# Performance work log

Measured on AMD Instinct MI355X. Metric: run time of the kernel, lower is better.

## Reference

```python
import jax, jax.numpy as jnp
import numpy as np

N, D = 8192, 4096


def setup_inputs() -> dict:
    key = jax.random.key(0)
    k1, k2, k3 = jax.random.split(key, 3)
    x = jax.random.normal(k1, (N, D), jnp.float32)
    W = jax.random.normal(k2, (D, D), jnp.float32) / np.sqrt(D)  # nn.Linear weight [out,in]
    b = jax.random.normal(k3, (D,), jnp.float32) * 0.01
    recency_weight = jnp.full((1,), -0.1, jnp.float32)
    return {"x": x, "W": W, "b": b, "recency_weight": recency_weight}


def reference(x, W, b, recency_weight):
    # linear -> relu projection
    x_proj = jax.nn.relu(x @ W.T + b)  # [N, D]
    # self-similarity
    scores = x_proj @ x_proj.T  # [N, N]
    n = scores.shape[0]
    idx = jnp.arange(n)
    # triu mask with diagonal=0 (use_current_timestep=False): keep strictly lower triangle
    mask = idx[None, :] >= idx[:, None]
    scores = jnp.where(mask, -jnp.inf, scores)
    # recency bias: toeplitz(arange(n)) == |i - j|, zeroed on masked positions
    rec = jnp.abs(idx[:, None] - idx[None, :]).astype(scores.dtype)
    rec = jnp.where(mask, 0.0, rec)
    scores = scores + recency_weight[0] * rec
    # row 0 is fully masked (-inf everywhere); replace with finite values to avoid
    # NaN in softmax -- the row is overwritten with zeros afterwards anyway.
    scores = scores.at[0].set(0.0)
    attn = jax.nn.softmax(scores, axis=1)
    attn = attn.at[0].set(0.0)  # matches scores[0] = zeros in the torch code
    return attn
```

## Files before the change

kernel.cpp:

```cpp
#include <hip/hip_runtime.h>
#include <hip/hip_bf16.h>
#include <stdint.h>

typedef _Float16 f16_t;
typedef f16_t f16x8_t __attribute__((ext_vector_type(8)));
typedef f16_t f16x4_t __attribute__((ext_vector_type(4)));
typedef float f32x4_t __attribute__((ext_vector_type(4)));

#define NROWS 8192
#define DDIM  4096
#define BK 32
#define KTILES (DDIM / BK)
#define LSTR 40

__device__ __forceinline__ void gload16(const void* g, void* s) {
  __builtin_amdgcn_global_load_lds(
      (const __attribute__((address_space(1))) void*)g,
      (__attribute__((address_space(3))) void*)s, 16, 0, 0);
}

__global__ __launch_bounds__(256) void k_split(const float* __restrict__ in,
                                               f16_t* __restrict__ hi,
                                               f16_t* __restrict__ lo) {
  const long i = ((long)blockIdx.x * 256 + threadIdx.x) * 4;
  const float4 v = *reinterpret_cast<const float4*>(in + i);
  float vv[4] = {v.x, v.y, v.z, v.w};
  f16x4_t h, l;
#pragma unroll
  for (int c = 0; c < 4; ++c) {
    f16_t hh = (f16_t)vv[c];
    h[c] = hh;
    l[c] = (f16_t)(vv[c] - (float)hh);
  }
  *reinterpret_cast<f16x4_t*>(hi + i) = h;
  *reinterpret_cast<f16x4_t*>(lo + i) = l;
}

typedef f16_t lds4_t[4][256][BK];

__device__ __forceinline__ void gemm_core256_3p(
    const f16_t* __restrict__ pAh, const f16_t* __restrict__ pAl, long lda,
    const f16_t* __restrict__ pBh, const f16_t* __restrict__ pBl, long ldb,
    lds4_t* sm, f32x4_t (&acc)[8][4]) {
  const int t = threadIdx.x, lane = t & 63, w = t >> 6;
  const int fr = lane & 15, kg = lane >> 4;
  const int wr = (w >> 2) * 128, wc = (w & 3) * 64;
  const int w32 = w * 32;
  const int sr0 = w32 + (lane >> 2);
  const int sg = (((lane & 3) ^ ((lane >> 3) & 3)) * 8);
  const int kge = (kg ^ ((fr >> 1) & 3)) * 8;

#pragma unroll
  for (int m = 0; m < 8; ++m)
#pragma unroll
    for (int n = 0; n < 4; ++n) acc[m][n] = f32x4_t{0.f, 0.f, 0.f, 0.f};

  const f16_t* gAh = pAh + (long)sr0 * lda + sg;
  const f16_t* gAl = pAl + (long)sr0 * lda + sg;
  const f16_t* gBh = pBh + (long)sr0 * ldb + sg;
  const f16_t* gBl = pBl + (long)sr0 * ldb + sg;
  const long a16 = 16 * lda, b16 = 16 * ldb;

  auto issue = [&](int buf, int plane, const f16_t* g, long ld16, int k0) {
    gload16(g + k0, &sm[buf][plane][w32][0]);
    gload16(g + ld16 + k0, &sm[buf][plane][w32 + 16][0]);
  };

  f16x8_t ah[8], al[8], bh[4], bl[4];
  auto read8 = [&](f16x8_t(&R)[8], int buf, int plane) {
#pragma unroll
    for (int m = 0; m < 8; ++m)
      R[m] = *reinterpret_cast<const f16x8_t*>(&sm[buf][plane][wr + m * 16 + fr][kge]);
  };
  auto read4 = [&](f16x8_t(&R)[4], int buf, int plane) {
#pragma unroll
    for (int n = 0; n < 4; ++n)
      R[n] = *reinterpret_cast<const f16x8_t*>(&sm[buf][plane][wc + n * 16 + fr][kge]);
  };
  auto mfma32 = [&](f16x8_t(&A)[8], f16x8_t(&B)[4]) {
    __builtin_amdgcn_s_setprio(1);
#pragma unroll
    for (int m = 0; m < 8; ++m)
#pragma unroll
      for (int n = 0; n < 4; ++n)
        acc[m][n] = __builtin_amdgcn_mfma_f32_16x16x32_f16(A[m], B[n], acc[m][n], 0, 0, 0);
    __builtin_amdgcn_s_setprio(0);
  };

  issue(0, 0, gAh, a16, 0);
  issue(0, 2, gBh, b16, 0);
  issue(0, 3, gBl, b16, 0);
  issue(0, 1, gAl, a16, 0);
  asm volatile("s_waitcnt vmcnt(4)" ::: "memory");
  __builtin_amdgcn_s_barrier();

  for (int kt = 0; kt < KTILES - 1; ++kt) {
    const int c = kt & 1;
    const int k0 = (kt + 1) * BK;
    read8(ah, c, 0);
    read4(bh, c, 2);
    issue(c ^ 1, 0, gAh, a16, k0);
    issue(c ^ 1, 2, gBh, b16, k0);
    __builtin_amdgcn_s_barrier();
    mfma32(ah, bh);
    asm volatile("s_waitcnt vmcnt(6)" ::: "memory");
    __builtin_amdgcn_s_barrier();
    read4(bl, c, 3);
    issue(c ^ 1, 3, gBl, b16, k0);
    __builtin_amdgcn_s_barrier();
    mfma32(ah, bl);
    asm volatile("s_waitcnt vmcnt(6)" ::: "memory");
    __builtin_amdgcn_s_barrier();
    read8(al, c, 1);
    issue(c ^ 1, 1, gAl, a16, k0);
    __builtin_amdgcn_s_barrier();
    mfma32(al, bh);
    asm volatile("s_waitcnt vmcnt(4)" ::: "memory");
    __builtin_amdgcn_s_barrier();
  }
  {
    const int c = (KTILES - 1) & 1;
    read8(ah, c, 0);
    read4(bh, c, 2);
    __builtin_amdgcn_s_barrier();
    mfma32(ah, bh);
    asm volatile("s_waitcnt vmcnt(2)" ::: "memory");
    __builtin_amdgcn_s_barrier();
    read4(bl, c, 3);
    __builtin_amdgcn_s_barrier();
    mfma32(ah, bl);
    asm volatile("s_waitcnt vmcnt(0)" ::: "memory");
    __builtin_amdgcn_s_barrier();
    read8(al, c, 1);
    mfma32(al, bh);
  }
}

typedef f16_t lds3_t[3][256][BK];

__device__ __forceinline__ void gemm_core256_2p(
    const f16_t* __restrict__ pAh, long lda,
    const f16_t* __restrict__ pBh, const f16_t* __restrict__ pBl, long ldb,
    lds3_t* sm, f32x4_t (&acc)[8][4]) {
  const int t = threadIdx.x, lane = t & 63, w = t >> 6;
  const int fr = lane & 15, kg = lane >> 4;
  const int wr = (w >> 2) * 128, wc = (w & 3) * 64;
  const int w32 = w * 32;
  const int sr0 = w32 + (lane >> 2);
  const int sg = (((lane & 3) ^ ((lane >> 3) & 3)) * 8);
  const int kge = (kg ^ ((fr >> 1) & 3)) * 8;

#pragma unroll
  for (int m = 0; m < 8; ++m)
#pragma unroll
    for (int n = 0; n < 4; ++n) acc[m][n] = f32x4_t{0.f, 0.f, 0.f, 0.f};

  const f16_t* gAh = pAh + (long)sr0 * lda + sg;
  const f16_t* gBh = pBh + (long)sr0 * ldb + sg;
  const f16_t* gBl = pBl + (long)sr0 * ldb + sg;
  const long a16 = 16 * lda, b16 = 16 * ldb;

  auto issue = [&](int buf, int plane, const f16_t* g, long ld16, int k0) {
    gload16(g + k0, &sm[buf][plane][w32][0]);
    gload16(g + ld16 + k0, &sm[buf][plane][w32 + 16][0]);
  };

  f16x8_t ah[8], bh[4], bl[4];
  auto read8 = [&](f16x8_t(&R)[8], int buf, int plane) {
#pragma unroll
    for (int m = 0; m < 8; ++m)
      R[m] = *reinterpret_cast<const f16x8_t*>(&sm[buf][plane][wr + m * 16 + fr][kge]);
  };
  auto read4 = [&](f16x8_t(&R)[4], int buf, int plane) {
#pragma unroll
    for (int n = 0; n < 4; ++n)
      R[n] = *reinterpret_cast<const f16x8_t*>(&sm[buf][plane][wc + n * 16 + fr][kge]);
  };
  auto mfma32 = [&](f16x8_t(&A)[8], f16x8_t(&B)[4]) {
    __builtin_amdgcn_s_setprio(1);
#pragma unroll
    for (int m = 0; m < 8; ++m)
#pragma unroll
      for (int n = 0; n < 4; ++n)
        acc[m][n] = __builtin_amdgcn_mfma_f32_16x16x32_f16(A[m], B[n], acc[m][n], 0, 0, 0);
    __builtin_amdgcn_s_setprio(0);
  };

  issue(0, 0, gAh, a16, 0);
  issue(0, 1, gBh, b16, 0);
  issue(0, 2, gBl, b16, 0);
  asm volatile("s_waitcnt vmcnt(2)" ::: "memory");
  __builtin_amdgcn_s_barrier();

  for (int kt = 0; kt < KTILES - 1; ++kt) {
    const int c = kt & 1;
    const int k0 = (kt + 1) * BK;
    read8(ah, c, 0);
    read4(bh, c, 1);
    issue(c ^ 1, 0, gAh, a16, k0);
    issue(c ^ 1, 1, gBh, b16, k0);
    __builtin_amdgcn_s_barrier();
    mfma32(ah, bh);
    asm volatile("s_waitcnt vmcnt(4)" ::: "memory");
    __builtin_amdgcn_s_barrier();
    read4(bl, c, 2);
    issue(c ^ 1, 2, gBl, b16, k0);
    __builtin_amdgcn_s_barrier();
    mfma32(ah, bl);
    asm volatile("s_waitcnt vmcnt(2)" ::: "memory");
    __builtin_amdgcn_s_barrier();
  }
  {
    const int c = (KTILES - 1) & 1;
    read8(ah, c, 0);
    read4(bh, c, 1);
    __builtin_amdgcn_s_barrier();
    mfma32(ah, bh);
    asm volatile("s_waitcnt vmcnt(0)" ::: "memory");
    __builtin_amdgcn_s_barrier();
    read4(bl, c, 2);
    mfma32(ah, bl);
  }
}

__global__ __launch_bounds__(512, 2) void k_gemm1_256(
    const f16_t* __restrict__ xh, const f16_t* __restrict__ xl,
    const f16_t* __restrict__ Wh, const f16_t* __restrict__ Wl,
    const float* __restrict__ bias,
    f16_t* __restrict__ xph, f16_t* __restrict__ xpl) {
  extern __shared__ char smraw[];
  lds4_t* sm = (lds4_t*)smraw;

  int bid = (int)blockIdx.x;
  bid = (bid & 7) * 64 + (bid >> 3);
  const int bx = bid & 15, by = bid >> 4;
  const long brow = (long)by * 256, bcol = (long)bx * 256;

  f32x4_t acc[8][4];
  gemm_core256_3p(xh + brow * DDIM, xl + brow * DDIM, DDIM,
                  Wh + bcol * DDIM, Wl + bcol * DDIM, DDIM, sm, acc);

  const int t = threadIdx.x, lane = t & 63, w = t >> 6;
  const int wr = (w >> 2) * 128, wc = (w & 3) * 64;
  const int cr = (lane >> 4) * 4, cc = lane & 15;
#pragma unroll
  for (int n = 0; n < 4; ++n) {
    const long col = bcol + wc + n * 16 + cc;
    const float bb = bias[col];
#pragma unroll
    for (int m = 0; m < 8; ++m) {
      const long row0 = brow + wr + m * 16 + cr;
#pragma unroll
      for (int r = 0; r < 4; ++r) {
        const float v = fmaxf(acc[m][n][r] + bb, 0.f);
        const f16_t h = (f16_t)v;
        xph[(row0 + r) * (long)DDIM + col] = h;
        xpl[(row0 + r) * (long)DDIM + col] = (f16_t)(v - (float)h);
      }
    }
  }
}

__global__ __launch_bounds__(512, 2) void k_gemm2_256(
    const f16_t* __restrict__ xph, const f16_t* __restrict__ xpl,
    const float* __restrict__ rwp, float* __restrict__ out) {
  extern __shared__ char smraw[];
  lds3_t* sm = (lds3_t*)smraw;

  int bid = (int)blockIdx.x;
  bid = (bid & 7) * 66 + (bid >> 3);
  int by = (int)((sqrtf(8.f * (float)bid + 1.f) - 1.f) * 0.5f);
  while ((by + 1) * (by + 2) / 2 <= bid) ++by;
  while (by * (by + 1) / 2 > bid) --by;
  const int bx = bid - by * (by + 1) / 2;

  const long brow = (long)by * 256, bcol = (long)bx * 256;
  f32x4_t acc[8][4];
  gemm_core256_2p(xph + brow * DDIM, DDIM,
                  xph + bcol * DDIM, xpl + bcol * DDIM, DDIM, sm, acc);

  const float rw = rwp[0];
  const int t = threadIdx.x, lane = t & 63, w = t >> 6;
  const int wr = (w >> 2) * 128, wc = (w & 3) * 64;
  const int cr = (lane >> 4) * 4, cc = lane & 15;
#pragma unroll
  for (int n = 0; n < 4; ++n) {
    const long gj = bcol + wc + n * 16 + cc;
#pragma unroll
    for (int m = 0; m < 8; ++m) {
      const long gi0 = brow + wr + m * 16 + cr;
#pragma unroll
      for (int r = 0; r < 4; ++r) {
        const long gi = gi0 + r;
        out[gi * (long)NROWS + gj] = acc[m][n][r] + rw * (float)(gi - gj);
      }
    }
  }
}

__device__ __forceinline__ void stage_split(const float* __restrict__ src, long ld,
                                            f16_t (&hi)[128][LSTR],
                                            f16_t (&lo)[128][LSTR],
                                            int t) {
#pragma unroll
  for (int i = 0; i < 4; ++i) {
    const int f = i * 256 + t;
    const int row = f >> 3;
    const int kq = (f & 7) << 2;
    const float4 v = *reinterpret_cast<const float4*>(src + (long)row * ld + kq);
    float vv[4] = {v.x, v.y, v.z, v.w};
    f16x4_t h, l;
#pragma unroll
    for (int c = 0; c < 4; ++c) {
      f16_t hh = (f16_t)vv[c];
      h[c] = hh;
      l[c] = (f16_t)(vv[c] - (float)hh);
    }
    *reinterpret_cast<f16x4_t*>(&hi[row][kq]) = h;
    *reinterpret_cast<f16x4_t*>(&lo[row][kq]) = l;
  }
}

__global__ __launch_bounds__(256) void k_gemm1_slow(
    const float* __restrict__ x, const float* __restrict__ W,
    const float* __restrict__ bias,
    f16_t* __restrict__ xph, f16_t* __restrict__ xpl) {
  __shared__ alignas(16) f16_t Ahi[128][LSTR];
  __shared__ alignas(16) f16_t Alo[128][LSTR];
  __shared__ alignas(16) f16_t Bhi[128][LSTR];
  __shared__ alignas(16) f16_t Blo[128][LSTR];

  const long brow = (long)blockIdx.y * 128;
  const long bcol = (long)blockIdx.x * 128;
  const int t = threadIdx.x, lane = t & 63;
  const int wr = ((t >> 6) >> 1) * 64, wc = ((t >> 6) & 1) * 64;
  const int fr = lane & 15, kg = lane >> 4;

  f32x4_t acc[4][4];
#pragma unroll
  for (int m = 0; m < 4; ++m)
#pragma unroll
    for (int n = 0; n < 4; ++n) acc[m][n] = f32x4_t{0.f, 0.f, 0.f, 0.f};

  const float* Abase = x + brow * DDIM;
  const float* Bbase = W + bcol * DDIM;
  for (int k0 = 0; k0 < DDIM; k0 += BK) {
    __syncthreads();
    stage_split(Abase + k0, DDIM, Ahi, Alo, t);
    stage_split(Bbase + k0, DDIM, Bhi, Blo, t);
    __syncthreads();

    f16x8_t ah[4], al[4], bh[4], bl[4];
#pragma unroll
    for (int m = 0; m < 4; ++m) {
      ah[m] = *reinterpret_cast<const f16x8_t*>(&Ahi[wr + m * 16 + fr][kg * 8]);
      al[m] = *reinterpret_cast<const f16x8_t*>(&Alo[wr + m * 16 + fr][kg * 8]);
      bh[m] = *reinterpret_cast<const f16x8_t*>(&Bhi[wc + m * 16 + fr][kg * 8]);
      bl[m] = *reinterpret_cast<const f16x8_t*>(&Blo[wc + m * 16 + fr][kg * 8]);
    }
#pragma unroll
    for (int m = 0; m < 4; ++m)
#pragma unroll
      for (int n = 0; n < 4; ++n) {
        acc[m][n] = __builtin_amdgcn_mfma_f32_16x16x32_f16(ah[m], bh[n], acc[m][n], 0, 0, 0);
        acc[m][n] = __builtin_amdgcn_mfma_f32_16x16x32_f16(ah[m], bl[n], acc[m][n], 0, 0, 0);
        acc[m][n] = __builtin_amdgcn_mfma_f32_16x16x32_f16(al[m], bh[n], acc[m][n], 0, 0, 0);
      }
  }

  const int cr = (lane >> 4) * 4, cc = lane & 15;
#pragma unroll
  for (int n = 0; n < 4; ++n) {
    const long col = bcol + wc + n * 16 + cc;
    const float bb = bias[col];
#pragma unroll
    for (int m = 0; m < 4; ++m) {
      const long row0 = brow + wr + m * 16 + cr;
#pragma unroll
      for (int r = 0; r < 4; ++r) {
        const float v = fmaxf(acc[m][n][r] + bb, 0.f);
        const f16_t h = (f16_t)v;
        xph[(row0 + r) * (long)DDIM + col] = h;
        xpl[(row0 + r) * (long)DDIM + col] = (f16_t)(v - (float)h);
      }
    }
  }
}

__global__ __launch_bounds__(256) void k_row_softmax(float* __restrict__ out, int n) {
  const int i = blockIdx.x;
  float* row = out + (size_t)i * n;
  const int L = i;
  const int t = threadIdx.x;
  __shared__ float red[4];

  float m = -3.402823466e+38f;
  for (int j = t; j < L; j += 256) m = fmaxf(m, row[j]);
#pragma unroll
  for (int o = 32; o > 0; o >>= 1) m = fmaxf(m, __shfl_down(m, o, 64));
  if ((t & 63) == 0) red[t >> 6] = m;
  __syncthreads();
  m = fmaxf(fmaxf(red[0], red[1]), fmaxf(red[2], red[3]));
  __syncthreads();

  float s = 0.f;
  for (int j = t; j < L; j += 256) s += expf(row[j] - m);
#pragma unroll
  for (int o = 32; o > 0; o >>= 1) s += __shfl_down(s, o, 64);
  if ((t & 63) == 0) red[t >> 6] = s;
  __syncthreads();
  s = red[0] + red[1] + red[2] + red[3];
  const float inv = (L > 0) ? 1.f / s : 0.f;

  for (int j = t; j < n; j += 256) {
    row[j] = (j < L) ? expf(row[j] - m) * inv : 0.f;
  }
}

extern "C" void kernel_launch(void* const* d_in, const int* in_sizes, int n_in,
                              void* d_out, int out_size, void* d_ws, size_t ws_size,
                              hipStream_t stream) {
  (void)in_sizes; (void)n_in; (void)out_size;
  const float* x = (const float*)d_in[0];
  const float* W = (const float*)d_in[1];
  const float* b = (const float*)d_in[2];
  const float* rw = (const float*)d_in[3];
  float* out = (float*)d_out;

  const size_t NX = (size_t)NROWS * DDIM;
  const size_t NW = (size_t)DDIM * DDIM;
  char* ws = (char*)d_ws;
  f16_t* xph = (f16_t*)ws;
  f16_t* xpl = (f16_t*)(ws + NX * 2);

  const int LDSB1 = 2 * 4 * 256 * BK * 2;
  const int LDSB2 = 2 * 3 * 256 * BK * 2;
  (void)hipFuncSetAttribute(reinterpret_cast<const void*>(k_gemm1_256),
                            hipFuncAttributeMaxDynamicSharedMemorySize, LDSB1);
  (void)hipFuncSetAttribute(reinterpret_cast<const void*>(k_gemm2_256),
                            hipFuncAttributeMaxDynamicSharedMemorySize, LDSB2);

  const size_t need_full = NX * 4  + NX * 4  + NW * 4 ;
  if (ws_size >= need_full) {
    f16_t* xh = (f16_t*)(ws + NX * 4);
    f16_t* xl = (f16_t*)(ws + NX * 6);
    f16_t* Wh = (f16_t*)(ws + NX * 8);
    f16_t* Wl = (f16_t*)(ws + NX * 8 + NW * 2);
    k_split<<<(int)(NX / 1024), 256, 0, stream>>>(x, xh, xl);
    k_split<<<(int)(NW / 1024), 256, 0, stream>>>(W, Wh, Wl);
    k_gemm1_256<<<512, 512, LDSB1, stream>>>(xh, xl, Wh, Wl, b, xph, xpl);
  } else {
    k_gemm1_slow<<<dim3(DDIM / 128, NROWS / 128), 256, 0, stream>>>(x, W, b, xph, xpl);
  }

  const int ntri = (NROWS / 256) * (NROWS / 256 + 1) / 2;
  k_gemm2_256<<<ntri, 512, LDSB2, stream>>>(xph, xpl, rw, out);
  k_row_softmax<<<NROWS, 256, 0, stream>>>(out, NROWS);
}
```

Measured before the change: 1.408 ms.

## Reschedule GEMM pipelines, skip masked diagonal warps, use online softmax

The two GEMM main loops are reordered so that global-to-LDS loads for the next tile are issued before the LDS reads. Several block barriers are replaced by explicit lgkmcnt waits. In the second GEMM, diagonal tiles skip the MFMA work for the upper-right warp quadrant, which is entirely masked. The row softmax becomes a single-pass online max/sum that uses fast __expf, removing one read pass over each row. The trade-offs are a risk of LDS race hazards from the removed barriers and slightly lower exp precision.

Measured after the change: 1.422 ms. About the same (+1.0%).

```diff
diff --git a/kernel.cpp b/kernel.cpp
--- a/kernel.cpp
+++ b/kernel.cpp
@@ -38,7 +38,7 @@
 
 typedef f16_t lds4_t[4][256][BK];
 
-__device__ __forceinline__ void gemm_core256_3p(
+__device__ __forceinline__ void gemm_core256_g1(
     const f16_t* __restrict__ pAh, const f16_t* __restrict__ pAl, long lda,
     const f16_t* __restrict__ pBh, const f16_t* __restrict__ pBl, long ldb,
     lds4_t* sm, f32x4_t (&acc)[8][4]) {
@@ -91,57 +91,52 @@
   issue(0, 2, gBh, b16, 0);
   issue(0, 3, gBl, b16, 0);
   issue(0, 1, gAl, a16, 0);
-  asm volatile("s_waitcnt vmcnt(4)" ::: "memory");
+  asm volatile("s_waitcnt vmcnt(0)" ::: "memory");
   __builtin_amdgcn_s_barrier();
 
   for (int kt = 0; kt < KTILES - 1; ++kt) {
     const int c = kt & 1;
     const int k0 = (kt + 1) * BK;
+    issue(c ^ 1, 0, gAh, a16, k0);
+    issue(c ^ 1, 2, gBh, b16, k0);
+    issue(c ^ 1, 3, gBl, b16, k0);
     read8(ah, c, 0);
     read4(bh, c, 2);
-    issue(c ^ 1, 0, gAh, a16, k0);
-    issue(c ^ 1, 2, gBh, b16, k0);
-    __builtin_amdgcn_s_barrier();
+    read4(bl, c, 3);
+    asm volatile("s_waitcnt lgkmcnt(0)" ::: "memory");
     mfma32(ah, bh);
-    asm volatile("s_waitcnt vmcnt(6)" ::: "memory");
-    __builtin_amdgcn_s_barrier();
-    read4(bl, c, 3);
-    issue(c ^ 1, 3, gBl, b16, k0);
-    __builtin_amdgcn_s_barrier();
     mfma32(ah, bl);
     asm volatile("s_waitcnt vmcnt(6)" ::: "memory");
     __builtin_amdgcn_s_barrier();
     read8(al, c, 1);
     issue(c ^ 1, 1, gAl, a16, k0);
-    __builtin_amdgcn_s_barrier();
+    asm volatile("s_waitcnt lgkmcnt(0)" ::: "memory");
     mfma32(al, bh);
-    asm volatile("s_waitcnt vmcnt(4)" ::: "memory");
+    asm volatile("s_waitcnt vmcnt(2)" ::: "memory");
     __builtin_amdgcn_s_barrier();
   }
   {
     const int c = (KTILES - 1) & 1;
     read8(ah, c, 0);
     read4(bh, c, 2);
-    __builtin_amdgcn_s_barrier();
+    read4(bl, c, 3);
+    asm volatile("s_waitcnt lgkmcnt(0)" ::: "memory");
     mfma32(ah, bh);
-    asm volatile("s_waitcnt vmcnt(2)" ::: "memory");
-    __builtin_amdgcn_s_barrier();
-    read4(bl, c, 3);
-    __builtin_amdgcn_s_barrier();
     mfma32(ah, bl);
     asm volatile("s_waitcnt vmcnt(0)" ::: "memory");
     __builtin_amdgcn_s_barrier();
     read8(al, c, 1);
+    asm volatile("s_waitcnt lgkmcnt(0)" ::: "memory");
     mfma32(al, bh);
   }
 }
 
 typedef f16_t lds3_t[3][256][BK];
 
-__device__ __forceinline__ void gemm_core256_2p(
+__device__ __forceinline__ void gemm_core256_g2(
     const f16_t* __restrict__ pAh, long lda,
     const f16_t* __restrict__ pBh, const f16_t* __restrict__ pBl, long ldb,
-    lds3_t* sm, f32x4_t (&acc)[8][4]) {
+    lds3_t* sm, f32x4_t (&acc)[8][4], bool diag) {
   const int t = threadIdx.x, lane = t & 63, w = t >> 6;
   const int fr = lane & 15, kg = lane >> 4;
   const int wr = (w >> 2) * 128, wc = (w & 3) * 64;
@@ -149,6 +144,7 @@
   const int sr0 = w32 + (lane >> 2);
   const int sg = (((lane & 3) ^ ((lane >> 3) & 3)) * 8);
   const int kge = (kg ^ ((fr >> 1) & 3)) * 8;
+  const bool skipw = diag && (wr == 0) && (wc >= 128);
 
 #pragma unroll
   for (int m = 0; m < 8; ++m)
@@ -189,37 +185,48 @@
   issue(0, 0, gAh, a16, 0);
   issue(0, 1, gBh, b16, 0);
   issue(0, 2, gBl, b16, 0);
-  asm volatile("s_waitcnt vmcnt(2)" ::: "memory");
+  asm volatile("s_waitcnt vmcnt(0)" ::: "memory");
   __builtin_amdgcn_s_barrier();
 
   for (int kt = 0; kt < KTILES - 1; ++kt) {
     const int c = kt & 1;
     const int k0 = (kt + 1) * BK;
-    read8(ah, c, 0);
-    read4(bh, c, 1);
     issue(c ^ 1, 0, gAh, a16, k0);
     issue(c ^ 1, 1, gBh, b16, k0);
-    __builtin_amdgcn_s_barrier();
-    mfma32(ah, bh);
+    if (!skipw) {
+      read8(ah, c, 0);
+      read4(bh, c, 1);
+      asm volatile("s_waitcnt lgkmcnt(0)" ::: "memory");
+      mfma32(ah, bh);
+    }
     asm volatile("s_waitcnt vmcnt(4)" ::: "memory");
     __builtin_amdgcn_s_barrier();
-    read4(bl, c, 2);
+    if (!skipw) {
+      read4(bl, c, 2);
+    }
     issue(c ^ 1, 2, gBl, b16, k0);
-    __builtin_amdgcn_s_barrier();
-    mfma32(ah, bl);
+    if (!skipw) {
+      asm volatile("s_waitcnt lgkmcnt(0)" ::: "memory");
+      mfma32(ah, bl);
+    }
     asm volatile("s_waitcnt vmcnt(2)" ::: "memory");
     __builtin_amdgcn_s_barrier();
   }
   {
     const int c = (KTILES - 1) & 1;
-    read8(ah, c, 0);
-    read4(bh, c, 1);
-    __builtin_amdgcn_s_barrier();
-    mfma32(ah, bh);
+    if (!skipw) {
+      read8(ah, c, 0);
+      read4(bh, c, 1);
+      asm volatile("s_waitcnt lgkmcnt(0)" ::: "memory");
+      mfma32(ah, bh);
+    }
     asm volatile("s_waitcnt vmcnt(0)" ::: "memory");
     __builtin_amdgcn_s_barrier();
-    read4(bl, c, 2);
-    mfma32(ah, bl);
+    if (!skipw) {
+      read4(bl, c, 2);
+      asm volatile("s_waitcnt lgkmcnt(0)" ::: "memory");
+      mfma32(ah, bl);
+    }
   }
 }
 
@@ -237,7 +244,7 @@
   const long brow = (long)by * 256, bcol = (long)bx * 256;
 
   f32x4_t acc[8][4];
-  gemm_core256_3p(xh + brow * DDIM, xl + brow * DDIM, DDIM,
+  gemm_core256_g1(xh + brow * DDIM, xl + brow * DDIM, DDIM,
                   Wh + bcol * DDIM, Wl + bcol * DDIM, DDIM, sm, acc);
 
   const int t = threadIdx.x, lane = t & 63, w = t >> 6;
@@ -276,8 +283,8 @@
 
   const long brow = (long)by * 256, bcol = (long)bx * 256;
   f32x4_t acc[8][4];
-  gemm_core256_2p(xph + brow * DDIM, DDIM,
-                  xph + bcol * DDIM, xpl + bcol * DDIM, DDIM, sm, acc);
+  gemm_core256_g2(xph + brow * DDIM, DDIM,
+                  xph + bcol * DDIM, xpl + bcol * DDIM, DDIM, sm, acc, bx == by);
 
   const float rw = rwp[0];
   const int t = threadIdx.x, lane = t & 63, w = t >> 6;
@@ -392,28 +399,32 @@
   float* row = out + (size_t)i * n;
   const int L = i;
   const int t = threadIdx.x;
-  __shared__ float red[4];
-
-  float m = -3.402823466e+38f;
-  for (int j = t; j < L; j += 256) m = fmaxf(m, row[j]);
-#pragma unroll
-  for (int o = 32; o > 0; o >>= 1) m = fmaxf(m, __shfl_down(m, o, 64));
-  if ((t & 63) == 0) red[t >> 6] = m;
+  __shared__ float redm[4], reds[4];
+
+  float m = -3.0e38f, s = 0.f;
+  for (int j = t; j < L; j += 256) {
+    const float v = row[j];
+    const float M = fmaxf(m, v);
+    s = s * __expf(m - M) + __expf(v - M);
+    m = M;
+  }
+#pragma unroll
+  for (int o = 32; o > 0; o >>= 1) {
+    const float om = __shfl_down(m, o, 64);
+    const float os = __shfl_down(s, o, 64);
+    const float M = fmaxf(m, om);
+    s = s * __expf(m - M) + os * __expf(om - M);
+    m = M;
+  }
+  if ((t & 63) == 0) { redm[t >> 6] = m; reds[t >> 6] = s; }
   __syncthreads();
-  m = fmaxf(fmaxf(red[0], red[1]), fmaxf(red[2], red[3]));
-  __syncthreads();
-
-  float s = 0.f;
-  for (int j = t; j < L; j += 256) s += expf(row[j] - m);
-#pragma unroll
-  for (int o = 32; o > 0; o >>= 1) s += __shfl_down(s, o, 64);
-  if ((t & 63) == 0) red[t >> 6] = s;
-  __syncthreads();
-  s = red[0] + red[1] + red[2] + red[3];
-  const float inv = (L > 0) ? 1.f / s : 0.f;
+  const float M4 = fmaxf(fmaxf(redm[0], redm[1]), fmaxf(redm[2], redm[3]));
+  const float S4 = reds[0] * __expf(redm[0] - M4) + reds[1] * __expf(redm[1] - M4) +
+                   reds[2] * __expf(redm[2] - M4) + reds[3] * __expf(redm[3] - M4);
+  const float inv = (L > 0) ? 1.f / S4 : 0.f;
 
   for (int j = t; j < n; j += 256) {
-    row[j] = (j < L) ? expf(row[j] - m) * inv : 0.f;
+    row[j] = (j < L) ? __expf(row[j] - M4) * inv : 0.f;
   }
 }
 
```
